# Kernel optimization log

Measured on AMD Instinct MI355X. Metric: run time of the kernel, lower is better.

The kernel has to match this reference:

```python
import jax, jax.numpy as jnp
import numpy as np

N = 100000        # nodes
E = 1600000       # edges (avg degree 16)
H = 128           # gnn_hidden_size
F_NODE = 4        # node_features (forced to 4 by _validate_and_fix_data)
F_EDGE = 2        # edge_features (forced to 2)
L = 3             # gnn_layers
BN_EPS = 1e-5
NORM_EPS = 1e-12


def _sage_layer(h, src, dst, eattr, Wn, Ws, gamma, beta):
    # message: lin_neighbor(concat(x_j, edge_attr)) where x_j = h[src]
    msg = jnp.concatenate([h[src], eattr], axis=-1) @ Wn          # [E+N, H]
    agg = jax.ops.segment_sum(msg, dst, num_segments=N)           # scatter-sum
    cnt = jax.ops.segment_sum(jnp.ones(dst.shape[0], h.dtype), dst, num_segments=N)
    agg = agg / jnp.maximum(cnt, 1.0)[:, None]                    # mean aggregation
    out = jax.nn.relu(agg + h @ Ws)                               # self-loop linear + ReLU
    # BatchNorm1d (batch statistics, biased var)
    mean = out.mean(axis=0)
    var = out.var(axis=0)
    out = (out - mean) * jax.lax.rsqrt(var + BN_EPS) * gamma + beta
    # dropout = identity (eval); L2 normalize per node
    nrm = jnp.maximum(jnp.linalg.norm(out, axis=-1, keepdims=True), NORM_EPS)
    return out / nrm


def setup_inputs() -> dict:
    key = jax.random.key(0)
    ks = jax.random.split(key, 24)
    s = 0.05
    inp = {
        "x": jax.random.normal(ks[0], (N, F_NODE), jnp.float32),
        "edge_index": jax.random.randint(ks[1], (2, E), 0, N, dtype=jnp.int32),
        "edge_attr": jax.random.uniform(ks[2], (E, F_EDGE), jnp.float32),
        "W_in": jax.random.normal(ks[3], (F_NODE, H), jnp.float32) * s,
        "b_in": jnp.zeros((H,), jnp.float32),
        "W_jump": jax.random.normal(ks[4], (L * H, H), jnp.float32) * s,
        "b_jump": jnp.zeros((H,), jnp.float32),
        "W1": jax.random.normal(ks[5], (H, H // 2), jnp.float32) * s,
        "b1": jnp.zeros((H // 2,), jnp.float32),
        "W2": jax.random.normal(ks[6], (H // 2, 1), jnp.float32) * s,
        "b2": jnp.zeros((1,), jnp.float32),
    }
    for l in range(L):
        inp[f"Wn_{l}"] = jax.random.normal(ks[7 + 4 * l], (H + F_EDGE, H), jnp.float32) * s
        inp[f"Ws_{l}"] = jax.random.normal(ks[8 + 4 * l], (H, H), jnp.float32) * s
        inp[f"gamma_{l}"] = jnp.ones((H,), jnp.float32)
        inp[f"beta_{l}"] = jnp.zeros((H,), jnp.float32)
    return inp


def reference(x, edge_index, edge_attr, W_in, b_in,
              Wn_0, Ws_0, gamma_0, beta_0,
              Wn_1, Ws_1, gamma_1, beta_1,
              Wn_2, Ws_2, gamma_2, beta_2,
              W_jump, b_jump, W1, b1, W2, b2):
    # add self loops (with zero edge_attr), as in _safe_add_self_loops
    loop = jnp.arange(N, dtype=edge_index.dtype)
    src = jnp.concatenate([edge_index[0], loop])
    dst = jnp.concatenate([edge_index[1], loop])
    eattr = jnp.concatenate([edge_attr, jnp.zeros((N, F_EDGE), edge_attr.dtype)], axis=0)

    h = x @ W_in + b_in                                          # input_projection
    layer_params = [(Wn_0, Ws_0, gamma_0, beta_0),
                    (Wn_1, Ws_1, gamma_1, beta_1),
                    (Wn_2, Ws_2, gamma_2, beta_2)]
    layer_outputs = []
    for Wn, Ws, gamma, beta in layer_params:
        h = _sage_layer(h, src, dst, eattr, Wn, Ws, gamma, beta)
        layer_outputs.append(h)
    # jump (skip) connection: concat all layer outputs -> Linear -> ReLU
    h = jax.nn.relu(jnp.concatenate(layer_outputs, axis=-1) @ W_jump + b_jump)
    # neighbor_scorer: Linear -> ReLU -> Linear -> scalar per node
    scores = jax.nn.relu(h @ W1 + b1) @ W2 + b2                  # [N, 1]
    return scores[:, 0]
```

## Files before the change

kernel.cpp:

```cpp
#include <hip/hip_runtime.h>


#define HDIM 128

using f16x8 = __attribute__((ext_vector_type(8))) _Float16;
using f32x4 = __attribute__((ext_vector_type(4))) float;

__device__ inline unsigned pack_f16x2(float a, float b) {
  _Float16 ha = (_Float16)a, hb = (_Float16)b;
  unsigned short ua = __builtin_bit_cast(unsigned short, ha);
  unsigned short ub = __builtin_bit_cast(unsigned short, hb);
  return (unsigned)ua | ((unsigned)ub << 16);
}
__device__ inline float2 unpack_f16x2(unsigned u) {
  _Float16 lo = __builtin_bit_cast(_Float16, (unsigned short)(u & 0xffffu));
  _Float16 hi = __builtin_bit_cast(_Float16, (unsigned short)(u >> 16));
  return make_float2((float)lo, (float)hi);
}

__global__ __launch_bounds__(256) void count_kernel(
    const int* __restrict__ dst, int* __restrict__ cnt,
    int* __restrict__ rank, int E) {
  int e = blockIdx.x * 256 + threadIdx.x;
  if (e >= E) return;
  rank[e] = atomicAdd(&cnt[dst[e]], 1);
}

__global__ __launch_bounds__(128) void scan_block_sum(
    const int* __restrict__ cnt, int* __restrict__ bsum, int N) {
  __shared__ int sd[128];
  int t = threadIdx.x;
  int i = blockIdx.x * 128 + t;
  sd[t] = (i < N) ? cnt[i] : 0;
  __syncthreads();
  for (int off = 64; off > 0; off >>= 1) {
    if (t < off) sd[t] += sd[t + off];
    __syncthreads();
  }
  if (t == 0) bsum[blockIdx.x] = sd[0];
}

__global__ __launch_bounds__(256) void scan_partials(
    const int* __restrict__ bsum, int* __restrict__ boff, int nch) {
  __shared__ int sd[256];
  int t = threadIdx.x;
  int base = t * 4;
  int v0 = (base + 0 < nch) ? bsum[base + 0] : 0;
  int v1 = (base + 1 < nch) ? bsum[base + 1] : 0;
  int v2 = (base + 2 < nch) ? bsum[base + 2] : 0;
  int v3 = (base + 3 < nch) ? bsum[base + 3] : 0;
  sd[t] = v0 + v1 + v2 + v3;
  __syncthreads();
  for (int off = 1; off < 256; off <<= 1) {
    int x = sd[t];
    int y = (t >= off) ? sd[t - off] : 0;
    __syncthreads();
    sd[t] = x + y;
    __syncthreads();
  }
  int run = (t == 0) ? 0 : sd[t - 1];
  if (base + 0 < nch) boff[base + 0] = run; run += v0;
  if (base + 1 < nch) boff[base + 1] = run; run += v1;
  if (base + 2 < nch) boff[base + 2] = run; run += v2;
  if (base + 3 < nch) boff[base + 3] = run;
}

__global__ __launch_bounds__(128) void scan_final(
    const int* __restrict__ cnt, const int* __restrict__ boff,
    int* __restrict__ rs, int N) {
  __shared__ int sd[128];
  int t = threadIdx.x, b = blockIdx.x;
  int i = b * 128 + t;
  int v = (i < N) ? cnt[i] : 0;
  sd[t] = v;
  __syncthreads();
  for (int off = 1; off < 128; off <<= 1) {
    int x = sd[t];
    int y = (t >= off) ? sd[t - off] : 0;
    __syncthreads();
    sd[t] = x + y;
    __syncthreads();
  }
  if (i < N) rs[i] = boff[b] + ((t == 0) ? 0 : sd[t - 1]);
}

__global__ __launch_bounds__(256) void fill_kernel(
    const int* __restrict__ src, const int* __restrict__ dst,
    const float* __restrict__ ea, const int* __restrict__ rs,
    const int* __restrict__ rank, uint2* __restrict__ cidx2, int E) {
  int e = blockIdx.x * 256 + threadIdx.x;
  if (e >= E) return;
  int d = dst[e];
  float2 v = *reinterpret_cast<const float2*>(&ea[2 * (size_t)e]);
  int pos = rs[d] + rank[e];
  cidx2[pos] = make_uint2((unsigned)src[e], pack_f16x2(v.x, v.y));
}

__global__ __launch_bounds__(256) void aggx_kernel(
    const float* __restrict__ x, const int* __restrict__ rs,
    const int* __restrict__ cnt, const uint2* __restrict__ cidx2,
    float* __restrict__ aggx, float* __restrict__ eagg, int N) {
  int i = blockIdx.x * 256 + threadIdx.x;
  if (i >= N) return;
  float4 a = *reinterpret_cast<const float4*>(&x[(size_t)i * 4]);
  float4 b = make_float4(0.f, 0.f, 0.f, 0.f);
  float e0 = 0.f, e1 = 0.f, f0 = 0.f, f1 = 0.f;
  int p = rs[i], e = p + cnt[i];
  for (; p + 1 < e; p += 2) {
    uint2 c0 = cidx2[p], c1 = cidx2[p + 1];
    float4 v0 = *reinterpret_cast<const float4*>(&x[(size_t)c0.x * 4]);
    float4 v1 = *reinterpret_cast<const float4*>(&x[(size_t)c1.x * 4]);
    float2 u0 = unpack_f16x2(c0.y);
    float2 u1 = unpack_f16x2(c1.y);
    a.x += v0.x; a.y += v0.y; a.z += v0.z; a.w += v0.w;
    b.x += v1.x; b.y += v1.y; b.z += v1.z; b.w += v1.w;
    e0 += u0.x; e1 += u0.y;
    f0 += u1.x; f1 += u1.y;
  }
  if (p < e) {
    uint2 c0 = cidx2[p];
    float4 v0 = *reinterpret_cast<const float4*>(&x[(size_t)c0.x * 4]);
    float2 u0 = unpack_f16x2(c0.y);
    a.x += v0.x; a.y += v0.y; a.z += v0.z; a.w += v0.w;
    e0 += u0.x; e1 += u0.y;
  }
  a.x += b.x; a.y += b.y; a.z += b.z; a.w += b.w;
  *reinterpret_cast<float4*>(&aggx[(size_t)i * 4]) = a;
  eagg[2 * (size_t)i + 0] = e0 + f0;
  eagg[2 * (size_t)i + 1] = e1 + f1;
}

__global__ __launch_bounds__(256) void pack_weights_kernel(
    const float* __restrict__ Wn0, const float* __restrict__ Ws0,
    const float* __restrict__ Wn1, const float* __restrict__ Ws1,
    const float* __restrict__ Wn2, const float* __restrict__ Ws2,
    const float* __restrict__ Wj, _Float16* __restrict__ outp) {
  int i = blockIdx.x * 256 + threadIdx.x;
  if (i >= 147456) return;
  int j = i & 7, lane = (i >> 3) & 63;
  float v;
  if (i < 98304) {
    int l = i >> 15;
    int r = i & 32767;
    int nt = (r >> 9) & 7, kt = r >> 12;
    int k = kt * 32 + (lane >> 4) * 8 + j;
    int n = nt * 16 + (lane & 15);
    const float* Wn = (l == 0) ? Wn0 : (l == 1) ? Wn1 : Wn2;
    const float* Ws = (l == 0) ? Ws0 : (l == 1) ? Ws1 : Ws2;
    v = (k < 128) ? Wn[(size_t)k * HDIM + n] : Ws[(size_t)(k - 128) * HDIM + n];
  } else {
    int r = i - 98304;
    int nt = (r >> 9) & 7, kt = r >> 12;
    int k = kt * 32 + (lane >> 4) * 8 + j;
    int n = nt * 16 + (lane & 15);
    v = Wj[(size_t)k * HDIM + n];
  }
  outp[i] = (_Float16)v;
}

template <bool L0>
__global__ __launch_bounds__(256) void sage_mfma_kernel(
    const float* __restrict__ A0f, const float* __restrict__ A1f,
    const _Float16* __restrict__ Hprev, const int* __restrict__ rs,
    const uint2* __restrict__ cidx2,
    const float* __restrict__ Wi, const float* __restrict__ bi,
    const float* __restrict__ eagg, const int* __restrict__ cnt,
    const _Float16* __restrict__ Bp, const float* __restrict__ Wn,
    _Float16* __restrict__ outh, float* __restrict__ bnstat, int N) {
  __shared__ _Float16 sA[64 * 256];
  __shared__ float sE[128];
  __shared__ float sBNs[4][128];
  __shared__ float sBNq[4][128];
  const int t = threadIdx.x;
  const int base = blockIdx.x * 64;

  if (t < 64) {
    int grow = base + t;
    float e0 = 0.f, e1 = 0.f;
    if (grow < N) {
      float inv = 1.0f / ((float)cnt[grow] + 1.0f);
      e0 = eagg[2 * (size_t)grow] * inv;
      e1 = eagg[2 * (size_t)grow + 1] * inv;
    }
    sE[2 * t] = e0;
    sE[2 * t + 1] = e1;
  }

  if (L0) {
#pragma unroll
    for (int it = 0; it < 8; ++it) {
      int c = t + it * 256;
      int row = c >> 5, k8 = c & 31;
      int grow = base + row;
      f16x8 hv = {};
      if (grow < N) {
        float inv = 1.0f / ((float)cnt[grow] + 1.0f);
        float scale = (k8 < 16) ? inv : 1.0f;
        const float* rp = (k8 < 16) ? &A0f[(size_t)grow * 4] : &A1f[(size_t)grow * 4];
        float4 r = *reinterpret_cast<const float4*>(rp);
        int col0 = (k8 & 15) * 8;
#pragma unroll
        for (int jj = 0; jj < 8; ++jj) {
          int col = col0 + jj;
          hv[jj] = (_Float16)(bi[col] + scale * (r.x * Wi[col] + r.y * Wi[HDIM + col] +
                                                 r.z * Wi[2 * HDIM + col] + r.w * Wi[3 * HDIM + col]));
        }
      }
      int byte = (row * 512 + k8 * 16) ^ ((row & 7) << 4);
      *reinterpret_cast<f16x8*>(reinterpret_cast<char*>(sA) + byte) = hv;
    }
  } else {
    const int row = t >> 2, q = t & 3;
    const int grow = base + row;
    float acc[32];
#pragma unroll
    for (int c = 0; c < 32; ++c) acc[c] = 0.f;
    f16x8 selfv[4] = {};
    if (grow < N) {
      const f16x8* selfp = reinterpret_cast<const f16x8*>(Hprev + (size_t)grow * HDIM) + q * 4;
#pragma unroll
      for (int j = 0; j < 4; ++j) {
        selfv[j] = selfp[j];
#pragma unroll
        for (int jj = 0; jj < 8; ++jj) acc[j * 8 + jj] = (float)selfv[j][jj];
      }
      int p = rs[grow];
      int e = p + cnt[grow];
      for (; p + 1 < e; p += 2) {
        uint2 q0 = cidx2[p], q1 = cidx2[p + 1];
        const f16x8* n0 = reinterpret_cast<const f16x8*>(Hprev + (size_t)q0.x * HDIM) + q * 4;
        const f16x8* n1 = reinterpret_cast<const f16x8*>(Hprev + (size_t)q1.x * HDIM) + q * 4;
        f16x8 c0[4], c1[4];
#pragma unroll
        for (int j = 0; j < 4; ++j) c0[j] = n0[j];
#pragma unroll
        for (int j = 0; j < 4; ++j) c1[j] = n1[j];
#pragma unroll
        for (int j = 0; j < 4; ++j)
#pragma unroll
          for (int jj = 0; jj < 8; ++jj)
            acc[j * 8 + jj] += (float)c0[j][jj] + (float)c1[j][jj];
      }
      if (p < e) {
        uint2 q0 = cidx2[p];
        const f16x8* n0 = reinterpret_cast<const f16x8*>(Hprev + (size_t)q0.x * HDIM) + q * 4;
#pragma unroll
        for (int j = 0; j < 4; ++j) {
          f16x8 c0 = n0[j];
#pragma unroll
          for (int jj = 0; jj < 8; ++jj) acc[j * 8 + jj] += (float)c0[jj];
        }
      }
      float inv = 1.0f / ((float)cnt[grow] + 1.0f);
#pragma unroll
      for (int c = 0; c < 32; ++c) acc[c] *= inv;
    }
    const int swz = (row & 7) << 4;
#pragma unroll
    for (int j = 0; j < 4; ++j) {
      f16x8 av;
#pragma unroll
      for (int jj = 0; jj < 8; ++jj) av[jj] = (_Float16)acc[j * 8 + jj];
      int k8a = q * 4 + j;
      *reinterpret_cast<f16x8*>(reinterpret_cast<char*>(sA) +
                                ((row * 512 + k8a * 16) ^ swz)) = av;
      int k8h = 16 + q * 4 + j;
      *reinterpret_cast<f16x8*>(reinterpret_cast<char*>(sA) +
                                ((row * 512 + k8h * 16) ^ swz)) = selfv[j];
    }
  }
  __syncthreads();

  const int lane = t & 63;
  const int w = t >> 6;
  const int col16 = lane & 15;
  const int kgrp = lane >> 4;
  f32x4 acc[8];
#pragma unroll
  for (int nt = 0; nt < 8; ++nt) acc[nt] = (f32x4){0.f, 0.f, 0.f, 0.f};

  const int arow = w * 16 + col16;
  const int aswz = (arow & 7) << 4;
#pragma unroll
  for (int kt = 0; kt < 8; ++kt) {
    int abyte = (arow * 512 + kt * 64 + kgrp * 16) ^ aswz;
    f16x8 a = *reinterpret_cast<const f16x8*>(reinterpret_cast<const char*>(sA) + abyte);
    const f16x8* bp = reinterpret_cast<const f16x8*>(Bp) + (size_t)kt * 512 + lane;
#pragma unroll
    for (int nt = 0; nt < 8; ++nt) {
      f16x8 b = bp[nt * 64];
      acc[nt] = __builtin_amdgcn_mfma_f32_16x16x32_f16(a, b, acc[nt], 0, 0, 0);
    }
  }

#pragma unroll
  for (int nt = 0; nt < 8; ++nt) {
    int col = nt * 16 + col16;
    float we0 = Wn[(size_t)128 * HDIM + col];
    float we1 = Wn[(size_t)129 * HDIM + col];
    float s = 0.f, q = 0.f;
#pragma unroll
    for (int i = 0; i < 4; ++i) {
      int lr = w * 16 + kgrp * 4 + i;
      int row = base + lr;
      if (row < N) {
        float v = acc[nt][i] + sE[2 * lr] * we0 + sE[2 * lr + 1] * we1;
        v = fmaxf(v, 0.f);
        outh[(size_t)row * HDIM + col] = (_Float16)v;
        s += v;
        q += v * v;
      }
    }
    s += __shfl_xor(s, 16, 64);
    s += __shfl_xor(s, 32, 64);
    q += __shfl_xor(q, 16, 64);
    q += __shfl_xor(q, 32, 64);
    if (lane < 16) {
      sBNs[w][col] = s;
      sBNq[w][col] = q;
    }
  }
  __syncthreads();
  if (t < 128) {
    float s = sBNs[0][t] + sBNs[1][t] + sBNs[2][t] + sBNs[3][t];
    float q = sBNq[0][t] + sBNq[1][t] + sBNq[2][t] + sBNq[3][t];
    atomicAdd(&bnstat[t], s);
    atomicAdd(&bnstat[HDIM + t], q);
  }
}

__global__ __launch_bounds__(256) void bn_l2_kernel(
    const _Float16* __restrict__ outh, const float* __restrict__ stat,
    const float* __restrict__ gamma, const float* __restrict__ beta,
    float invN, _Float16* __restrict__ h, int N) {
  __shared__ float sAB[256];
  int t = threadIdx.x;
  if (t < 128) {
    float mean = stat[t] * invN;
    float var = stat[128 + t] * invN - mean * mean;
    float A = gamma[t] / sqrtf(var + 1e-5f);
    sAB[t] = A;
    sAB[128 + t] = beta[t] - mean * A;
  }
  __syncthreads();
  int i = blockIdx.x * 4 + (t >> 6);
  if (i >= N) return;
  int lane = t & 63;
  unsigned u = (reinterpret_cast<const unsigned*>(outh + (size_t)i * HDIM))[lane];
  float2 v = unpack_f16x2(u);
  float A0 = sAB[lane * 2 + 0], A1 = sAB[lane * 2 + 1];
  float B0 = sAB[128 + lane * 2 + 0], B1 = sAB[128 + lane * 2 + 1];
  float y0 = v.x * A0 + B0;
  float y1 = v.y * A1 + B1;
  float s = y0 * y0 + y1 * y1;
#pragma unroll
  for (int m = 32; m > 0; m >>= 1) s += __shfl_xor(s, m, 64);
  float inv = 1.0f / fmaxf(sqrtf(s), 1e-12f);
  (reinterpret_cast<unsigned*>(h + (size_t)i * HDIM))[lane] =
      pack_f16x2(y0 * inv, y1 * inv);
}

__global__ __launch_bounds__(256) void jump_mfma_kernel(
    const _Float16* __restrict__ h1, const _Float16* __restrict__ h2,
    const _Float16* __restrict__ h3, const _Float16* __restrict__ Bp,
    const float* __restrict__ bj, const float* __restrict__ W1p,
    const float* __restrict__ b1p, const float* __restrict__ W2p,
    const float* __restrict__ b2p, float* __restrict__ outp, int N) {
  __shared__ _Float16 sA[64 * 384];
  const int t = threadIdx.x;
  const int base = blockIdx.x * 64;

  const _Float16* hs[3] = {h1, h2, h3};
#pragma unroll
  for (int it = 0; it < 12; ++it) {
    int c = t + it * 256;
    int row = c / 48, k8 = c % 48;
    int grow = base + row;
    f16x8 hv = {};
    if (grow < N)
      hv = (reinterpret_cast<const f16x8*>(hs[k8 >> 4] + (size_t)grow * HDIM))[k8 & 15];
    int byte = (row * 768 + k8 * 16) ^ ((row & 7) << 4);
    *reinterpret_cast<f16x8*>(reinterpret_cast<char*>(sA) + byte) = hv;
  }
  __syncthreads();

  const int lane = t & 63;
  const int w = t >> 6;
  const int col16 = lane & 15;
  const int kgrp = lane >> 4;
  f32x4 acc[8];
#pragma unroll
  for (int nt = 0; nt < 8; ++nt) acc[nt] = (f32x4){0.f, 0.f, 0.f, 0.f};

  const int arow = w * 16 + col16;
  const int aswz = (arow & 7) << 4;
#pragma unroll
  for (int kt = 0; kt < 12; ++kt) {
    int abyte = (arow * 768 + kt * 64 + kgrp * 16) ^ aswz;
    f16x8 a = *reinterpret_cast<const f16x8*>(reinterpret_cast<const char*>(sA) + abyte);
    const f16x8* bp = reinterpret_cast<const f16x8*>(Bp) + (size_t)kt * 512 + lane;
#pragma unroll
    for (int nt = 0; nt < 8; ++nt) {
      f16x8 b = bp[nt * 64];
      acc[nt] = __builtin_amdgcn_mfma_f32_16x16x32_f16(a, b, acc[nt], 0, 0, 0);
    }
  }
  __syncthreads();

  float* sG = reinterpret_cast<float*>(sA);
  float* sS = sG + 64 * 128;
#pragma unroll
  for (int nt = 0; nt < 8; ++nt) {
    int col = nt * 16 + col16;
    float bb = bj[col];
#pragma unroll
    for (int i = 0; i < 4; ++i) {
      int lr = w * 16 + kgrp * 4 + i;
      sG[lr * 128 + col] = fmaxf(acc[nt][i] + bb, 0.f);
    }
  }
  __syncthreads();

  const int m = t & 63, grp = t >> 6;
  float a2[16];
#pragma unroll
  for (int i = 0; i < 16; ++i) a2[i] = b1p[m];
#pragma unroll 4
  for (int k = 0; k < 128; ++k) {
    float wv = W1p[(size_t)k * 64 + m];
#pragma unroll
    for (int i = 0; i < 16; ++i) a2[i] += sG[(grp * 16 + i) * 128 + k] * wv;
  }
#pragma unroll
  for (int i = 0; i < 16; ++i) sS[(grp * 16 + i) * 64 + m] = fmaxf(a2[i], 0.f);
  __syncthreads();

  if (t < 64) {
    int row = base + t;
    if (row < N) {
      float s = b2p[0];
#pragma unroll 8
      for (int mm = 0; mm < 64; ++mm) s += sS[t * 64 + mm] * W2p[mm];
      outp[row] = s;
    }
  }
}

extern "C" void kernel_launch(void* const* d_in, const int* in_sizes, int n_in,
                              void* d_out, int out_size, void* d_ws, size_t ws_size,
                              hipStream_t stream) {
  const float* x      = (const float*)d_in[0];
  const int*   ei     = (const int*)d_in[1];
  const float* eattr  = (const float*)d_in[2];
  const float* W_in   = (const float*)d_in[3];
  const float* b_in   = (const float*)d_in[4];
  const float* W_jump = (const float*)d_in[5];
  const float* b_jump = (const float*)d_in[6];
  const float* W1     = (const float*)d_in[7];
  const float* b1     = (const float*)d_in[8];
  const float* W2     = (const float*)d_in[9];
  const float* b2     = (const float*)d_in[10];
  const float* Wn[3] = {(const float*)d_in[11], (const float*)d_in[15], (const float*)d_in[19]};
  const float* Ws[3] = {(const float*)d_in[12], (const float*)d_in[16], (const float*)d_in[20]};
  const float* gm[3] = {(const float*)d_in[13], (const float*)d_in[17], (const float*)d_in[21]};
  const float* bt[3] = {(const float*)d_in[14], (const float*)d_in[18], (const float*)d_in[22]};

  const int N = in_sizes[0] / 4;
  const int E = in_sizes[2] / 2;
  const int* srcp = ei;
  const int* dstp = ei + (size_t)E;
  const int nch = (N + 127) / 128;
  const size_t nh = (size_t)N * HDIM;

  char* wsb = (char*)d_ws;
  size_t off = 0;
  auto carve = [&](size_t bytes) -> void* {
    void* p = wsb + off;
    off = (off + bytes + 255) & ~(size_t)255;
    return p;
  };
  _Float16* h1   = (_Float16*)carve(nh * 2);
  _Float16* h2   = (_Float16*)carve(nh * 2);
  _Float16* h3   = (_Float16*)carve(nh * 2);
  _Float16* outh = (_Float16*)carve(nh * 2);
  float*    aggx = (float*)carve((size_t)N * 4 * 4);
  float*    eagg = (float*)carve((size_t)N * 2 * 4);
  int*      cnt  = (int*)carve((size_t)N * 4);
  int*      rowstart = (int*)carve((size_t)N * 4);
  int*      rank     = (int*)carve((size_t)E * 4);
  uint2*    cidx2    = (uint2*)carve((size_t)E * 8);
  int*      bsum = (int*)carve(4096);
  int*      boff = (int*)carve(4096);
  float*    bnstat = (float*)carve(1024);
  _Float16* wpack  = (_Float16*)carve(147456 * 2);

  hipMemsetAsync(cnt, 0, (size_t)N * sizeof(int), stream);
  count_kernel<<<(E + 255) / 256, 256, 0, stream>>>(dstp, cnt, rank, E);
  pack_weights_kernel<<<(147456 + 255) / 256, 256, 0, stream>>>(
      Wn[0], Ws[0], Wn[1], Ws[1], Wn[2], Ws[2], W_jump, wpack);
  scan_block_sum<<<nch, 128, 0, stream>>>(cnt, bsum, N);
  scan_partials<<<1, 256, 0, stream>>>(bsum, boff, nch);
  scan_final<<<nch, 128, 0, stream>>>(cnt, boff, rowstart, N);
  fill_kernel<<<(E + 255) / 256, 256, 0, stream>>>(srcp, dstp, eattr, rowstart, rank, cidx2, E);

  const int gemm_grid = (N + 63) / 64;
  const float invN = 1.0f / (float)N;

  aggx_kernel<<<(N + 255) / 256, 256, 0, stream>>>(x, rowstart, cnt, cidx2, aggx, eagg, N);
  hipMemsetAsync(bnstat, 0, 256 * sizeof(float), stream);
  sage_mfma_kernel<true><<<gemm_grid, 256, 0, stream>>>(
      aggx, x, nullptr, rowstart, cidx2, W_in, b_in, eagg, cnt, wpack, Wn[0],
      outh, bnstat, N);
  bn_l2_kernel<<<(N + 3) / 4, 256, 0, stream>>>(outh, bnstat, gm[0], bt[0], invN, h1, N);

  _Float16* hbuf[3] = {h1, h2, h3};
  for (int l = 1; l < 3; ++l) {
    hipMemsetAsync(bnstat, 0, 256 * sizeof(float), stream);
    sage_mfma_kernel<false><<<gemm_grid, 256, 0, stream>>>(
        nullptr, nullptr, hbuf[l - 1], rowstart, cidx2, nullptr, nullptr, eagg, cnt,
        wpack + (size_t)l * 32768, Wn[l], outh, bnstat, N);
    bn_l2_kernel<<<(N + 3) / 4, 256, 0, stream>>>(outh, bnstat, gm[l], bt[l], invN, hbuf[l], N);
  }

  jump_mfma_kernel<<<gemm_grid, 256, 0, stream>>>(h1, h2, h3, wpack + 98304, b_jump,
                                                  W1, b1, W2, b2, (float*)d_out, N);
}
```

Baseline: 590.7 us.

## Restructure neighbor gather to half-wave per row with deeper unrolling

The aggregation phase of the SAGE kernel is remapped so that 32 lanes cooperatively load one 256-byte neighbor row as f16x4 pieces. Two rows are processed per wave, and up to 8 neighbor gathers are kept in flight per iteration. The old mapping had 4 threads per row, each loading 64 bytes with only 2 neighbors unrolled. Blocks shrink to 128 threads covering 32 rows, and each wave now fills only its own 16 MFMA rows, which lets the non-layer-0 path drop the block barrier. The aim is more memory-level parallelism and better-coalesced gathers, at the cost of more blocks and twice as many BN-stat atomics.

Measured after the change: 651.9 us. 1.1x slower.

```diff
diff --git a/kernel.cpp b/kernel.cpp
--- a/kernel.cpp
+++ b/kernel.cpp
@@ -4,6 +4,7 @@
 #define HDIM 128
 
 using f16x8 = __attribute__((ext_vector_type(8))) _Float16;
+using f16x4 = __attribute__((ext_vector_type(4))) _Float16;
 using f32x4 = __attribute__((ext_vector_type(4))) float;
 
 __device__ inline unsigned pack_f16x2(float a, float b) {
@@ -159,7 +160,7 @@
 }
 
 template <bool L0>
-__global__ __launch_bounds__(256) void sage_mfma_kernel(
+__global__ __launch_bounds__(128, 4) void sage_mfma_kernel(
     const float* __restrict__ A0f, const float* __restrict__ A1f,
     const _Float16* __restrict__ Hprev, const int* __restrict__ rs,
     const uint2* __restrict__ cidx2,
@@ -167,29 +168,32 @@
     const float* __restrict__ eagg, const int* __restrict__ cnt,
     const _Float16* __restrict__ Bp, const float* __restrict__ Wn,
     _Float16* __restrict__ outh, float* __restrict__ bnstat, int N) {
-  __shared__ _Float16 sA[64 * 256];
-  __shared__ float sE[128];
-  __shared__ float sBNs[4][128];
-  __shared__ float sBNq[4][128];
+  __shared__ _Float16 sA[32 * 256];
+  __shared__ float sE[64];
+  __shared__ float sBNs[2][128];
+  __shared__ float sBNq[2][128];
   const int t = threadIdx.x;
-  const int base = blockIdx.x * 64;
-
-  if (t < 64) {
-    int grow = base + t;
+  const int w = t >> 6;
+  const int lane = t & 63;
+  const int base = blockIdx.x * 32;
+
+  if (lane < 16) {
+    int row = w * 16 + lane;
+    int grow = base + row;
     float e0 = 0.f, e1 = 0.f;
     if (grow < N) {
       float inv = 1.0f / ((float)cnt[grow] + 1.0f);
       e0 = eagg[2 * (size_t)grow] * inv;
       e1 = eagg[2 * (size_t)grow + 1] * inv;
     }
-    sE[2 * t] = e0;
-    sE[2 * t + 1] = e1;
+    sE[2 * row] = e0;
+    sE[2 * row + 1] = e1;
   }
 
   if (L0) {
 #pragma unroll
     for (int it = 0; it < 8; ++it) {
-      int c = t + it * 256;
+      int c = t + it * 128;
       int row = c >> 5, k8 = c & 31;
       int grow = base + row;
       f16x8 hv = {};
@@ -209,70 +213,74 @@
       int byte = (row * 512 + k8 * 16) ^ ((row & 7) << 4);
       *reinterpret_cast<f16x8*>(reinterpret_cast<char*>(sA) + byte) = hv;
     }
+    __syncthreads();
   } else {
-    const int row = t >> 2, q = t & 3;
-    const int grow = base + row;
-    float acc[32];
-#pragma unroll
-    for (int c = 0; c < 32; ++c) acc[c] = 0.f;
-    f16x8 selfv[4] = {};
-    if (grow < N) {
-      const f16x8* selfp = reinterpret_cast<const f16x8*>(Hprev + (size_t)grow * HDIM) + q * 4;
-#pragma unroll
-      for (int j = 0; j < 4; ++j) {
-        selfv[j] = selfp[j];
-#pragma unroll
-        for (int jj = 0; jj < 8; ++jj) acc[j * 8 + jj] = (float)selfv[j][jj];
+    const int sub = lane >> 5;
+    const int sl = lane & 31;
+    const f16x4* hb = reinterpret_cast<const f16x4*>(Hprev) + sl;
+    char* sAb = reinterpret_cast<char*>(sA);
+#pragma unroll 2
+    for (int rp = 0; rp < 8; ++rp) {
+      int row = w * 16 + rp * 2 + sub;
+      int grow = base + row;
+      float a0 = 0.f, a1 = 0.f, a2 = 0.f, a3 = 0.f;
+      f16x4 selfv = {};
+      if (grow < N) {
+        selfv = hb[(size_t)grow * 32];
+        a0 = (float)selfv[0]; a1 = (float)selfv[1];
+        a2 = (float)selfv[2]; a3 = (float)selfv[3];
+        int p = rs[grow];
+        const int cn = cnt[grow];
+        int e = p + cn;
+        for (; p + 7 < e; p += 8) {
+          uint2 q0 = cidx2[p], q1 = cidx2[p + 1], q2 = cidx2[p + 2], q3 = cidx2[p + 3];
+          uint2 q4 = cidx2[p + 4], q5 = cidx2[p + 5], q6 = cidx2[p + 6], q7 = cidx2[p + 7];
+          f16x4 v0 = hb[(size_t)q0.x * 32];
+          f16x4 v1 = hb[(size_t)q1.x * 32];
+          f16x4 v2 = hb[(size_t)q2.x * 32];
+          f16x4 v3 = hb[(size_t)q3.x * 32];
+          f16x4 v4 = hb[(size_t)q4.x * 32];
+          f16x4 v5 = hb[(size_t)q5.x * 32];
+          f16x4 v6 = hb[(size_t)q6.x * 32];
+          f16x4 v7 = hb[(size_t)q7.x * 32];
+          a0 += (float)v0[0] + (float)v1[0] + (float)v2[0] + (float)v3[0] +
+                (float)v4[0] + (float)v5[0] + (float)v6[0] + (float)v7[0];
+          a1 += (float)v0[1] + (float)v1[1] + (float)v2[1] + (float)v3[1] +
+                (float)v4[1] + (float)v5[1] + (float)v6[1] + (float)v7[1];
+          a2 += (float)v0[2] + (float)v1[2] + (float)v2[2] + (float)v3[2] +
+                (float)v4[2] + (float)v5[2] + (float)v6[2] + (float)v7[2];
+          a3 += (float)v0[3] + (float)v1[3] + (float)v2[3] + (float)v3[3] +
+                (float)v4[3] + (float)v5[3] + (float)v6[3] + (float)v7[3];
+        }
+        for (; p + 3 < e; p += 4) {
+          uint2 q0 = cidx2[p], q1 = cidx2[p + 1], q2 = cidx2[p + 2], q3 = cidx2[p + 3];
+          f16x4 v0 = hb[(size_t)q0.x * 32];
+          f16x4 v1 = hb[(size_t)q1.x * 32];
+          f16x4 v2 = hb[(size_t)q2.x * 32];
+          f16x4 v3 = hb[(size_t)q3.x * 32];
+          a0 += (float)v0[0] + (float)v1[0] + (float)v2[0] + (float)v3[0];
+          a1 += (float)v0[1] + (float)v1[1] + (float)v2[1] + (float)v3[1];
+          a2 += (float)v0[2] + (float)v1[2] + (float)v2[2] + (float)v3[2];
+          a3 += (float)v0[3] + (float)v1[3] + (float)v2[3] + (float)v3[3];
+        }
+        for (; p < e; ++p) {
+          uint2 q0 = cidx2[p];
+          f16x4 v0 = hb[(size_t)q0.x * 32];
+          a0 += (float)v0[0]; a1 += (float)v0[1];
+          a2 += (float)v0[2]; a3 += (float)v0[3];
+        }
+        float inv = 1.0f / ((float)cn + 1.0f);
+        a0 *= inv; a1 *= inv; a2 *= inv; a3 *= inv;
       }
-      int p = rs[grow];
-      int e = p + cnt[grow];
-      for (; p + 1 < e; p += 2) {
-        uint2 q0 = cidx2[p], q1 = cidx2[p + 1];
-        const f16x8* n0 = reinterpret_cast<const f16x8*>(Hprev + (size_t)q0.x * HDIM) + q * 4;
-        const f16x8* n1 = reinterpret_cast<const f16x8*>(Hprev + (size_t)q1.x * HDIM) + q * 4;
-        f16x8 c0[4], c1[4];
-#pragma unroll
-        for (int j = 0; j < 4; ++j) c0[j] = n0[j];
-#pragma unroll
-        for (int j = 0; j < 4; ++j) c1[j] = n1[j];
-#pragma unroll
-        for (int j = 0; j < 4; ++j)
-#pragma unroll
-          for (int jj = 0; jj < 8; ++jj)
-            acc[j * 8 + jj] += (float)c0[j][jj] + (float)c1[j][jj];
-      }
-      if (p < e) {
-        uint2 q0 = cidx2[p];
-        const f16x8* n0 = reinterpret_cast<const f16x8*>(Hprev + (size_t)q0.x * HDIM) + q * 4;
-#pragma unroll
-        for (int j = 0; j < 4; ++j) {
-          f16x8 c0 = n0[j];
-#pragma unroll
-          for (int jj = 0; jj < 8; ++jj) acc[j * 8 + jj] += (float)c0[jj];
-        }
-      }
-      float inv = 1.0f / ((float)cnt[grow] + 1.0f);
-#pragma unroll
-      for (int c = 0; c < 32; ++c) acc[c] *= inv;
-    }
-    const int swz = (row & 7) << 4;
-#pragma unroll
-    for (int j = 0; j < 4; ++j) {
-      f16x8 av;
-#pragma unroll
-      for (int jj = 0; jj < 8; ++jj) av[jj] = (_Float16)acc[j * 8 + jj];
-      int k8a = q * 4 + j;
-      *reinterpret_cast<f16x8*>(reinterpret_cast<char*>(sA) +
-                                ((row * 512 + k8a * 16) ^ swz)) = av;
-      int k8h = 16 + q * 4 + j;
-      *reinterpret_cast<f16x8*>(reinterpret_cast<char*>(sA) +
-                                ((row * 512 + k8h * 16) ^ swz)) = selfv[j];
-    }
-  }
-  __syncthreads();
-
-  const int lane = t & 63;
-  const int w = t >> 6;
+      int swz = (row & 7) << 4;
+      f16x4 av;
+      av[0] = (_Float16)a0; av[1] = (_Float16)a1;
+      av[2] = (_Float16)a2; av[3] = (_Float16)a3;
+      *reinterpret_cast<f16x4*>(sAb + ((row * 512 + sl * 8) ^ swz)) = av;
+      *reinterpret_cast<f16x4*>(sAb + ((row * 512 + 256 + sl * 8) ^ swz)) = selfv;
+    }
+  }
+
   const int col16 = lane & 15;
   const int kgrp = lane >> 4;
   f32x4 acc[8];
@@ -322,8 +330,8 @@
   }
   __syncthreads();
   if (t < 128) {
-    float s = sBNs[0][t] + sBNs[1][t] + sBNs[2][t] + sBNs[3][t];
-    float q = sBNq[0][t] + sBNq[1][t] + sBNq[2][t] + sBNq[3][t];
+    float s = sBNs[0][t] + sBNs[1][t];
+    float q = sBNq[0][t] + sBNq[1][t];
     atomicAdd(&bnstat[t], s);
     atomicAdd(&bnstat[HDIM + t], q);
   }
@@ -503,12 +511,12 @@
   scan_final<<<nch, 128, 0, stream>>>(cnt, boff, rowstart, N);
   fill_kernel<<<(E + 255) / 256, 256, 0, stream>>>(srcp, dstp, eattr, rowstart, rank, cidx2, E);
 
-  const int gemm_grid = (N + 63) / 64;
+  const int sage_grid = (N + 31) / 32;
   const float invN = 1.0f / (float)N;
 
   aggx_kernel<<<(N + 255) / 256, 256, 0, stream>>>(x, rowstart, cnt, cidx2, aggx, eagg, N);
   hipMemsetAsync(bnstat, 0, 256 * sizeof(float), stream);
-  sage_mfma_kernel<true><<<gemm_grid, 256, 0, stream>>>(
+  sage_mfma_kernel<true><<<sage_grid, 128, 0, stream>>>(
       aggx, x, nullptr, rowstart, cidx2, W_in, b_in, eagg, cnt, wpack, Wn[0],
       outh, bnstat, N);
   bn_l2_kernel<<<(N + 3) / 4, 256, 0, stream>>>(outh, bnstat, gm[0], bt[0], invN, h1, N);
@@ -516,12 +524,12 @@
   _Float16* hbuf[3] = {h1, h2, h3};
   for (int l = 1; l < 3; ++l) {
     hipMemsetAsync(bnstat, 0, 256 * sizeof(float), stream);
-    sage_mfma_kernel<false><<<gemm_grid, 256, 0, stream>>>(
+    sage_mfma_kernel<false><<<sage_grid, 128, 0, stream>>>(
         nullptr, nullptr, hbuf[l - 1], rowstart, cidx2, nullptr, nullptr, eagg, cnt,
         wpack + (size_t)l * 32768, Wn[l], outh, bnstat, N);
     bn_l2_kernel<<<(N + 3) / 4, 256, 0, stream>>>(outh, bnstat, gm[l], bt[l], invN, hbuf[l], N);
   }
 
-  jump_mfma_kernel<<<gemm_grid, 256, 0, stream>>>(h1, h2, h3, wpack + 98304, b_jump,
-                                                  W1, b1, W2, b2, (float*)d_out, N);
-}
+  jump_mfma_kernel<<<(N + 63) / 64, 256, 0, stream>>>(h1, h2, h3, wpack + 98304, b_jump,
+                                                      W1, b1, W2, b2, (float*)d_out, N);
+}
```

## Split neighbor gather into column-chunked kernel over transposed feature layout

Applied to the files above, without the earlier changes.

Node features are now stored in a chunk-transposed layout, with 8 chunks of 16 fp16 columns each. A new gather kernel aggregates neighbors one chunk at a time, so each chunk pass touches a 3.2 MB slice that can stay in cache, and it reads a compact int-only neighbor index. The SAGE GEMM kernel then only loads the precomputed mean aggregate and the self features, and the BN and jump kernels are adapted to the new layout. This adds an extra kernel launch per layer plus an extra aggregate buffer write and read, and the index array is read eight times.

Measured after the change: 740.3 us. 25.3% more time.

```diff
diff --git a/kernel.cpp b/kernel.cpp
--- a/kernel.cpp
+++ b/kernel.cpp
@@ -87,13 +87,16 @@
 __global__ __launch_bounds__(256) void fill_kernel(
     const int* __restrict__ src, const int* __restrict__ dst,
     const float* __restrict__ ea, const int* __restrict__ rs,
-    const int* __restrict__ rank, uint2* __restrict__ cidx2, int E) {
+    const int* __restrict__ rank, uint2* __restrict__ cidx2,
+    int* __restrict__ cidx1, int E) {
   int e = blockIdx.x * 256 + threadIdx.x;
   if (e >= E) return;
   int d = dst[e];
+  int s = src[e];
   float2 v = *reinterpret_cast<const float2*>(&ea[2 * (size_t)e]);
   int pos = rs[d] + rank[e];
-  cidx2[pos] = make_uint2((unsigned)src[e], pack_f16x2(v.x, v.y));
+  cidx2[pos] = make_uint2((unsigned)s, pack_f16x2(v.x, v.y));
+  cidx1[pos] = s;
 }
 
 __global__ __launch_bounds__(256) void aggx_kernel(
@@ -128,6 +131,61 @@
   *reinterpret_cast<float4*>(&aggx[(size_t)i * 4]) = a;
   eagg[2 * (size_t)i + 0] = e0 + f0;
   eagg[2 * (size_t)i + 1] = e1 + f1;
+}
+
+__global__ __launch_bounds__(256) void gatherT_kernel(
+    const _Float16* __restrict__ hT, const int* __restrict__ rs,
+    const int* __restrict__ cnt, const int* __restrict__ cidx1,
+    _Float16* __restrict__ aggT, int N) {
+  const int c = blockIdx.x & 7;
+  const int i = (blockIdx.x >> 3) * 256 + threadIdx.x;
+  if (i >= N) return;
+  const f16x8* hb = reinterpret_cast<const f16x8*>(hT) + (size_t)c * N * 2;
+  f16x8 s0 = hb[(size_t)i * 2];
+  f16x8 s1 = hb[(size_t)i * 2 + 1];
+  float acc[16];
+#pragma unroll
+  for (int j = 0; j < 8; ++j) {
+    acc[j] = (float)s0[j];
+    acc[8 + j] = (float)s1[j];
+  }
+  int p = rs[i];
+  const int cn = cnt[i];
+  int e = p + cn;
+  for (; p + 3 < e; p += 4) {
+    int n0 = __builtin_nontemporal_load(cidx1 + p);
+    int n1 = __builtin_nontemporal_load(cidx1 + p + 1);
+    int n2 = __builtin_nontemporal_load(cidx1 + p + 2);
+    int n3 = __builtin_nontemporal_load(cidx1 + p + 3);
+    f16x8 a0 = hb[(size_t)n0 * 2], a1 = hb[(size_t)n0 * 2 + 1];
+    f16x8 b0 = hb[(size_t)n1 * 2], b1 = hb[(size_t)n1 * 2 + 1];
+    f16x8 c0 = hb[(size_t)n2 * 2], c1 = hb[(size_t)n2 * 2 + 1];
+    f16x8 d0 = hb[(size_t)n3 * 2], d1 = hb[(size_t)n3 * 2 + 1];
+#pragma unroll
+    for (int j = 0; j < 8; ++j) {
+      acc[j] += ((float)a0[j] + (float)b0[j]) + ((float)c0[j] + (float)d0[j]);
+      acc[8 + j] += ((float)a1[j] + (float)b1[j]) + ((float)c1[j] + (float)d1[j]);
+    }
+  }
+  for (; p < e; ++p) {
+    int n0 = __builtin_nontemporal_load(cidx1 + p);
+    f16x8 a0 = hb[(size_t)n0 * 2], a1 = hb[(size_t)n0 * 2 + 1];
+#pragma unroll
+    for (int j = 0; j < 8; ++j) {
+      acc[j] += (float)a0[j];
+      acc[8 + j] += (float)a1[j];
+    }
+  }
+  float inv = 1.0f / ((float)cn + 1.0f);
+  f16x8 o0, o1;
+#pragma unroll
+  for (int j = 0; j < 8; ++j) {
+    o0[j] = (_Float16)(acc[j] * inv);
+    o1[j] = (_Float16)(acc[8 + j] * inv);
+  }
+  f16x8* op = reinterpret_cast<f16x8*>(aggT) + (size_t)c * N * 2 + (size_t)i * 2;
+  __builtin_nontemporal_store(o0, op);
+  __builtin_nontemporal_store(o1, op + 1);
 }
 
 __global__ __launch_bounds__(256) void pack_weights_kernel(
@@ -161,8 +219,7 @@
 template <bool L0>
 __global__ __launch_bounds__(256) void sage_mfma_kernel(
     const float* __restrict__ A0f, const float* __restrict__ A1f,
-    const _Float16* __restrict__ Hprev, const int* __restrict__ rs,
-    const uint2* __restrict__ cidx2,
+    const _Float16* __restrict__ AggT, const _Float16* __restrict__ HprevT,
     const float* __restrict__ Wi, const float* __restrict__ bi,
     const float* __restrict__ eagg, const int* __restrict__ cnt,
     const _Float16* __restrict__ Bp, const float* __restrict__ Wn,
@@ -210,63 +267,20 @@
       *reinterpret_cast<f16x8*>(reinterpret_cast<char*>(sA) + byte) = hv;
     }
   } else {
-    const int row = t >> 2, q = t & 3;
-    const int grow = base + row;
-    float acc[32];
-#pragma unroll
-    for (int c = 0; c < 32; ++c) acc[c] = 0.f;
-    f16x8 selfv[4] = {};
-    if (grow < N) {
-      const f16x8* selfp = reinterpret_cast<const f16x8*>(Hprev + (size_t)grow * HDIM) + q * 4;
-#pragma unroll
-      for (int j = 0; j < 4; ++j) {
-        selfv[j] = selfp[j];
-#pragma unroll
-        for (int jj = 0; jj < 8; ++jj) acc[j * 8 + jj] = (float)selfv[j][jj];
+#pragma unroll
+    for (int it = 0; it < 8; ++it) {
+      int idx = it * 256 + t;
+      int row = idx & 63, k8 = idx >> 6;
+      int grow = base + row;
+      f16x8 hv = {};
+      if (grow < N) {
+        int k = k8 & 15;
+        const _Float16* srcp = (k8 < 16) ? AggT : HprevT;
+        hv = *reinterpret_cast<const f16x8*>(
+            srcp + ((size_t)(k >> 1) * N + grow) * 16 + (k & 1) * 8);
       }
-      int p = rs[grow];
-      int e = p + cnt[grow];
-      for (; p + 1 < e; p += 2) {
-        uint2 q0 = cidx2[p], q1 = cidx2[p + 1];
-        const f16x8* n0 = reinterpret_cast<const f16x8*>(Hprev + (size_t)q0.x * HDIM) + q * 4;
-        const f16x8* n1 = reinterpret_cast<const f16x8*>(Hprev + (size_t)q1.x * HDIM) + q * 4;
-        f16x8 c0[4], c1[4];
-#pragma unroll
-        for (int j = 0; j < 4; ++j) c0[j] = n0[j];
-#pragma unroll
-        for (int j = 0; j < 4; ++j) c1[j] = n1[j];
-#pragma unroll
-        for (int j = 0; j < 4; ++j)
-#pragma unroll
-          for (int jj = 0; jj < 8; ++jj)
-            acc[j * 8 + jj] += (float)c0[j][jj] + (float)c1[j][jj];
-      }
-      if (p < e) {
-        uint2 q0 = cidx2[p];
-        const f16x8* n0 = reinterpret_cast<const f16x8*>(Hprev + (size_t)q0.x * HDIM) + q * 4;
-#pragma unroll
-        for (int j = 0; j < 4; ++j) {
-          f16x8 c0 = n0[j];
-#pragma unroll
-          for (int jj = 0; jj < 8; ++jj) acc[j * 8 + jj] += (float)c0[jj];
-        }
-      }
-      float inv = 1.0f / ((float)cnt[grow] + 1.0f);
-#pragma unroll
-      for (int c = 0; c < 32; ++c) acc[c] *= inv;
-    }
-    const int swz = (row & 7) << 4;
-#pragma unroll
-    for (int j = 0; j < 4; ++j) {
-      f16x8 av;
-#pragma unroll
-      for (int jj = 0; jj < 8; ++jj) av[jj] = (_Float16)acc[j * 8 + jj];
-      int k8a = q * 4 + j;
-      *reinterpret_cast<f16x8*>(reinterpret_cast<char*>(sA) +
-                                ((row * 512 + k8a * 16) ^ swz)) = av;
-      int k8h = 16 + q * 4 + j;
-      *reinterpret_cast<f16x8*>(reinterpret_cast<char*>(sA) +
-                                ((row * 512 + k8h * 16) ^ swz)) = selfv[j];
+      int byte = (row * 512 + k8 * 16) ^ ((row & 7) << 4);
+      *reinterpret_cast<f16x8*>(reinterpret_cast<char*>(sA) + byte) = hv;
     }
   }
   __syncthreads();
@@ -332,7 +346,7 @@
 __global__ __launch_bounds__(256) void bn_l2_kernel(
     const _Float16* __restrict__ outh, const float* __restrict__ stat,
     const float* __restrict__ gamma, const float* __restrict__ beta,
-    float invN, _Float16* __restrict__ h, int N) {
+    float invN, _Float16* __restrict__ hT, int N) {
   __shared__ float sAB[256];
   int t = threadIdx.x;
   if (t < 128) {
@@ -356,8 +370,8 @@
 #pragma unroll
   for (int m = 32; m > 0; m >>= 1) s += __shfl_xor(s, m, 64);
   float inv = 1.0f / fmaxf(sqrtf(s), 1e-12f);
-  (reinterpret_cast<unsigned*>(h + (size_t)i * HDIM))[lane] =
-      pack_f16x2(y0 * inv, y1 * inv);
+  size_t off = ((size_t)(lane >> 3) * N + i) * 16 + (lane & 7) * 2;
+  *reinterpret_cast<unsigned*>(hT + off) = pack_f16x2(y0 * inv, y1 * inv);
 }
 
 __global__ __launch_bounds__(256) void jump_mfma_kernel(
@@ -373,12 +387,15 @@
   const _Float16* hs[3] = {h1, h2, h3};
 #pragma unroll
   for (int it = 0; it < 12; ++it) {
-    int c = t + it * 256;
-    int row = c / 48, k8 = c % 48;
+    int idx = it * 256 + t;
+    int row = idx & 63, k8 = idx >> 6;
     int grow = base + row;
     f16x8 hv = {};
-    if (grow < N)
-      hv = (reinterpret_cast<const f16x8*>(hs[k8 >> 4] + (size_t)grow * HDIM))[k8 & 15];
+    if (grow < N) {
+      int kk = k8 & 15;
+      hv = *reinterpret_cast<const f16x8*>(
+          hs[k8 >> 4] + ((size_t)(kk >> 1) * N + grow) * 16 + (kk & 1) * 8);
+    }
     int byte = (row * 768 + k8 * 16) ^ ((row & 7) << 4);
     *reinterpret_cast<f16x8*>(reinterpret_cast<char*>(sA) + byte) = hv;
   }
@@ -483,12 +500,14 @@
   _Float16* h2   = (_Float16*)carve(nh * 2);
   _Float16* h3   = (_Float16*)carve(nh * 2);
   _Float16* outh = (_Float16*)carve(nh * 2);
+  _Float16* aggT = (_Float16*)carve(nh * 2);
   float*    aggx = (float*)carve((size_t)N * 4 * 4);
   float*    eagg = (float*)carve((size_t)N * 2 * 4);
   int*      cnt  = (int*)carve((size_t)N * 4);
   int*      rowstart = (int*)carve((size_t)N * 4);
   int*      rank     = (int*)carve((size_t)E * 4);
   uint2*    cidx2    = (uint2*)carve((size_t)E * 8);
+  int*      cidx1    = (int*)carve((size_t)E * 4);
   int*      bsum = (int*)carve(4096);
   int*      boff = (int*)carve(4096);
   float*    bnstat = (float*)carve(1024);
@@ -501,23 +520,26 @@
   scan_block_sum<<<nch, 128, 0, stream>>>(cnt, bsum, N);
   scan_partials<<<1, 256, 0, stream>>>(bsum, boff, nch);
   scan_final<<<nch, 128, 0, stream>>>(cnt, boff, rowstart, N);
-  fill_kernel<<<(E + 255) / 256, 256, 0, stream>>>(srcp, dstp, eattr, rowstart, rank, cidx2, E);
+  fill_kernel<<<(E + 255) / 256, 256, 0, stream>>>(srcp, dstp, eattr, rowstart, rank,
+                                                   cidx2, cidx1, E);
 
   const int gemm_grid = (N + 63) / 64;
+  const int gat_grid = 8 * ((N + 255) / 256);
   const float invN = 1.0f / (float)N;
 
   aggx_kernel<<<(N + 255) / 256, 256, 0, stream>>>(x, rowstart, cnt, cidx2, aggx, eagg, N);
   hipMemsetAsync(bnstat, 0, 256 * sizeof(float), stream);
   sage_mfma_kernel<true><<<gemm_grid, 256, 0, stream>>>(
-      aggx, x, nullptr, rowstart, cidx2, W_in, b_in, eagg, cnt, wpack, Wn[0],
+      aggx, x, nullptr, nullptr, W_in, b_in, eagg, cnt, wpack, Wn[0],
       outh, bnstat, N);
   bn_l2_kernel<<<(N + 3) / 4, 256, 0, stream>>>(outh, bnstat, gm[0], bt[0], invN, h1, N);
 
   _Float16* hbuf[3] = {h1, h2, h3};
   for (int l = 1; l < 3; ++l) {
+    gatherT_kernel<<<gat_grid, 256, 0, stream>>>(hbuf[l - 1], rowstart, cnt, cidx1, aggT, N);
     hipMemsetAsync(bnstat, 0, 256 * sizeof(float), stream);
     sage_mfma_kernel<false><<<gemm_grid, 256, 0, stream>>>(
-        nullptr, nullptr, hbuf[l - 1], rowstart, cidx2, nullptr, nullptr, eagg, cnt,
+        nullptr, nullptr, aggT, hbuf[l - 1], nullptr, nullptr, eagg, cnt,
         wpack + (size_t)l * 32768, Wn[l], outh, bnstat, N);
     bn_l2_kernel<<<(N + 3) / 4, 256, 0, stream>>>(outh, bnstat, gm[l], bt[l], invN, hbuf[l], N);
   }
```

## Sort CSR neighbor lists by source-index bucket for gather locality

Applied to the files above, without the earlier changes.

Counting is now done per (destination, source bucket) pair with 16 buckets of 8192 source ids. Each row's neighbors in the CSR are therefore grouped by source range, so the layer gather kernels read Hprev rows in roughly ascending address order, which should improve cache locality. The scan now covers 16N entries, a rowmeta kernel derives per-node counts, and the gather loop walks the 16 bucket boundaries. BN stat buffers are split per layer so one memset replaces three, in exchange for a heavier preprocessing scan and extra bounds reads in the inner loop.

Measured after the change: 710.4 us. 20.3% more time.

```diff
diff --git a/kernel.cpp b/kernel.cpp
--- a/kernel.cpp
+++ b/kernel.cpp
@@ -18,22 +18,35 @@
   return make_float2((float)lo, (float)hi);
 }
 
+__device__ inline int src_bucket(int s) {
+  int b = s >> 13;
+  return (b > 15) ? 15 : b;
+}
+
 __global__ __launch_bounds__(256) void count_kernel(
-    const int* __restrict__ dst, int* __restrict__ cnt,
-    int* __restrict__ rank, int E) {
+    const int* __restrict__ src, const int* __restrict__ dst,
+    int* __restrict__ cnt16, int* __restrict__ rank, int E) {
   int e = blockIdx.x * 256 + threadIdx.x;
   if (e >= E) return;
-  rank[e] = atomicAdd(&cnt[dst[e]], 1);
-}
-
-__global__ __launch_bounds__(128) void scan_block_sum(
-    const int* __restrict__ cnt, int* __restrict__ bsum, int N) {
-  __shared__ int sd[128];
+  int d = dst[e];
+  int s = src[e];
+  rank[e] = atomicAdd(&cnt16[((size_t)d << 4) + src_bucket(s)], 1);
+}
+
+__global__ __launch_bounds__(256) void scan_block_sum2048(
+    const int* __restrict__ a, int* __restrict__ bsum, int M) {
+  __shared__ int sd[256];
   int t = threadIdx.x;
-  int i = blockIdx.x * 128 + t;
-  sd[t] = (i < N) ? cnt[i] : 0;
-  __syncthreads();
-  for (int off = 64; off > 0; off >>= 1) {
+  int base = blockIdx.x * 2048 + t * 8;
+  int s = 0;
+#pragma unroll
+  for (int j = 0; j < 8; ++j) {
+    int i = base + j;
+    s += (i < M) ? a[i] : 0;
+  }
+  sd[t] = s;
+  __syncthreads();
+  for (int off = 128; off > 0; off >>= 1) {
     if (t < off) sd[t] += sd[t + off];
     __syncthreads();
   }
@@ -65,39 +78,63 @@
   if (base + 3 < nch) boff[base + 3] = run;
 }
 
-__global__ __launch_bounds__(128) void scan_final(
-    const int* __restrict__ cnt, const int* __restrict__ boff,
-    int* __restrict__ rs, int N) {
-  __shared__ int sd[128];
-  int t = threadIdx.x, b = blockIdx.x;
-  int i = b * 128 + t;
-  int v = (i < N) ? cnt[i] : 0;
-  sd[t] = v;
-  __syncthreads();
-  for (int off = 1; off < 128; off <<= 1) {
+__global__ __launch_bounds__(256) void scan_final2048(
+    const int* __restrict__ a, const int* __restrict__ boff,
+    int* __restrict__ outp, int M) {
+  __shared__ int sd[256];
+  int t = threadIdx.x;
+  int base = blockIdx.x * 2048 + t * 8;
+  int v[8];
+  int s = 0;
+#pragma unroll
+  for (int j = 0; j < 8; ++j) {
+    int i = base + j;
+    v[j] = (i < M) ? a[i] : 0;
+    s += v[j];
+  }
+  sd[t] = s;
+  __syncthreads();
+  for (int off = 1; off < 256; off <<= 1) {
     int x = sd[t];
     int y = (t >= off) ? sd[t - off] : 0;
     __syncthreads();
     sd[t] = x + y;
     __syncthreads();
   }
-  if (i < N) rs[i] = boff[b] + ((t == 0) ? 0 : sd[t - 1]);
+  int run = boff[blockIdx.x] + ((t == 0) ? 0 : sd[t - 1]);
+#pragma unroll
+  for (int j = 0; j < 8; ++j) {
+    int i = base + j;
+    if (i < M) outp[i] = run;
+    run += v[j];
+  }
+}
+
+__global__ __launch_bounds__(256) void rowmeta_kernel(
+    int* __restrict__ rs16, int* __restrict__ cnt, int N, int E) {
+  int i = blockIdx.x * 256 + threadIdx.x;
+  if (i >= N) return;
+  int start = rs16[(size_t)i << 4];
+  int end = (i == N - 1) ? E : rs16[((size_t)i << 4) + 16];
+  cnt[i] = end - start;
+  if (i == N - 1) rs16[(size_t)N << 4] = E;
 }
 
 __global__ __launch_bounds__(256) void fill_kernel(
     const int* __restrict__ src, const int* __restrict__ dst,
-    const float* __restrict__ ea, const int* __restrict__ rs,
+    const float* __restrict__ ea, const int* __restrict__ rs16,
     const int* __restrict__ rank, uint2* __restrict__ cidx2, int E) {
   int e = blockIdx.x * 256 + threadIdx.x;
   if (e >= E) return;
   int d = dst[e];
+  int s = src[e];
   float2 v = *reinterpret_cast<const float2*>(&ea[2 * (size_t)e]);
-  int pos = rs[d] + rank[e];
-  cidx2[pos] = make_uint2((unsigned)src[e], pack_f16x2(v.x, v.y));
+  int pos = rs16[((size_t)d << 4) + src_bucket(s)] + rank[e];
+  cidx2[pos] = make_uint2((unsigned)s, pack_f16x2(v.x, v.y));
 }
 
 __global__ __launch_bounds__(256) void aggx_kernel(
-    const float* __restrict__ x, const int* __restrict__ rs,
+    const float* __restrict__ x, const int* __restrict__ rs16,
     const int* __restrict__ cnt, const uint2* __restrict__ cidx2,
     float* __restrict__ aggx, float* __restrict__ eagg, int N) {
   int i = blockIdx.x * 256 + threadIdx.x;
@@ -105,7 +142,7 @@
   float4 a = *reinterpret_cast<const float4*>(&x[(size_t)i * 4]);
   float4 b = make_float4(0.f, 0.f, 0.f, 0.f);
   float e0 = 0.f, e1 = 0.f, f0 = 0.f, f1 = 0.f;
-  int p = rs[i], e = p + cnt[i];
+  int p = rs16[(size_t)i << 4], e = p + cnt[i];
   for (; p + 1 < e; p += 2) {
     uint2 c0 = cidx2[p], c1 = cidx2[p + 1];
     float4 v0 = *reinterpret_cast<const float4*>(&x[(size_t)c0.x * 4]);
@@ -161,7 +198,7 @@
 template <bool L0>
 __global__ __launch_bounds__(256) void sage_mfma_kernel(
     const float* __restrict__ A0f, const float* __restrict__ A1f,
-    const _Float16* __restrict__ Hprev, const int* __restrict__ rs,
+    const _Float16* __restrict__ Hprev, const int* __restrict__ rs16,
     const uint2* __restrict__ cidx2,
     const float* __restrict__ Wi, const float* __restrict__ bi,
     const float* __restrict__ eagg, const int* __restrict__ cnt,
@@ -224,31 +261,35 @@
 #pragma unroll
         for (int jj = 0; jj < 8; ++jj) acc[j * 8 + jj] = (float)selfv[j][jj];
       }
-      int p = rs[grow];
-      int e = p + cnt[grow];
-      for (; p + 1 < e; p += 2) {
-        uint2 q0 = cidx2[p], q1 = cidx2[p + 1];
-        const f16x8* n0 = reinterpret_cast<const f16x8*>(Hprev + (size_t)q0.x * HDIM) + q * 4;
-        const f16x8* n1 = reinterpret_cast<const f16x8*>(Hprev + (size_t)q1.x * HDIM) + q * 4;
-        f16x8 c0[4], c1[4];
-#pragma unroll
-        for (int j = 0; j < 4; ++j) c0[j] = n0[j];
-#pragma unroll
-        for (int j = 0; j < 4; ++j) c1[j] = n1[j];
-#pragma unroll
-        for (int j = 0; j < 4; ++j)
-#pragma unroll
-          for (int jj = 0; jj < 8; ++jj)
-            acc[j * 8 + jj] += (float)c0[j][jj] + (float)c1[j][jj];
-      }
-      if (p < e) {
-        uint2 q0 = cidx2[p];
-        const f16x8* n0 = reinterpret_cast<const f16x8*>(Hprev + (size_t)q0.x * HDIM) + q * 4;
-#pragma unroll
-        for (int j = 0; j < 4; ++j) {
-          f16x8 c0 = n0[j];
-#pragma unroll
-          for (int jj = 0; jj < 8; ++jj) acc[j * 8 + jj] += (float)c0[jj];
+      const int rbase = grow << 4;
+      int p = rs16[rbase];
+      for (int b = 1; b <= 16; ++b) {
+        int pe = rs16[rbase + b];
+        for (; p + 1 < pe; p += 2) {
+          uint2 q0 = cidx2[p], q1 = cidx2[p + 1];
+          const f16x8* m0 = reinterpret_cast<const f16x8*>(Hprev + (size_t)q0.x * HDIM) + q * 4;
+          const f16x8* m1 = reinterpret_cast<const f16x8*>(Hprev + (size_t)q1.x * HDIM) + q * 4;
+          f16x8 c0[4], c1[4];
+#pragma unroll
+          for (int j = 0; j < 4; ++j) c0[j] = m0[j];
+#pragma unroll
+          for (int j = 0; j < 4; ++j) c1[j] = m1[j];
+#pragma unroll
+          for (int j = 0; j < 4; ++j)
+#pragma unroll
+            for (int jj = 0; jj < 8; ++jj)
+              acc[j * 8 + jj] += (float)c0[j][jj] + (float)c1[j][jj];
+        }
+        if (p < pe) {
+          uint2 q0 = cidx2[p];
+          const f16x8* m0 = reinterpret_cast<const f16x8*>(Hprev + (size_t)q0.x * HDIM) + q * 4;
+#pragma unroll
+          for (int j = 0; j < 4; ++j) {
+            f16x8 c0 = m0[j];
+#pragma unroll
+            for (int jj = 0; jj < 8; ++jj) acc[j * 8 + jj] += (float)c0[jj];
+          }
+          p = pe;
         }
       }
       float inv = 1.0f / ((float)cnt[grow] + 1.0f);
@@ -469,8 +510,9 @@
   const int E = in_sizes[2] / 2;
   const int* srcp = ei;
   const int* dstp = ei + (size_t)E;
-  const int nch = (N + 127) / 128;
   const size_t nh = (size_t)N * HDIM;
+  const int M = 16 * N;
+  const int nch = (M + 2047) / 2048;
 
   char* wsb = (char*)d_ws;
   size_t off = 0;
@@ -486,40 +528,42 @@
   float*    aggx = (float*)carve((size_t)N * 4 * 4);
   float*    eagg = (float*)carve((size_t)N * 2 * 4);
   int*      cnt  = (int*)carve((size_t)N * 4);
-  int*      rowstart = (int*)carve((size_t)N * 4);
-  int*      rank     = (int*)carve((size_t)E * 4);
-  uint2*    cidx2    = (uint2*)carve((size_t)E * 8);
+  int*      cnt16 = (int*)carve((size_t)M * 4);
+  int*      rs16  = (int*)carve(((size_t)M + 16) * 4);
+  int*      rank  = (int*)carve((size_t)E * 4);
+  uint2*    cidx2 = (uint2*)carve((size_t)E * 8);
   int*      bsum = (int*)carve(4096);
   int*      boff = (int*)carve(4096);
-  float*    bnstat = (float*)carve(1024);
+  float*    bnstat = (float*)carve(3 * 256 * sizeof(float));
   _Float16* wpack  = (_Float16*)carve(147456 * 2);
 
-  hipMemsetAsync(cnt, 0, (size_t)N * sizeof(int), stream);
-  count_kernel<<<(E + 255) / 256, 256, 0, stream>>>(dstp, cnt, rank, E);
+  hipMemsetAsync(cnt16, 0, (size_t)M * sizeof(int), stream);
+  hipMemsetAsync(bnstat, 0, 3 * 256 * sizeof(float), stream);
+  count_kernel<<<(E + 255) / 256, 256, 0, stream>>>(srcp, dstp, cnt16, rank, E);
   pack_weights_kernel<<<(147456 + 255) / 256, 256, 0, stream>>>(
       Wn[0], Ws[0], Wn[1], Ws[1], Wn[2], Ws[2], W_jump, wpack);
-  scan_block_sum<<<nch, 128, 0, stream>>>(cnt, bsum, N);
+  scan_block_sum2048<<<nch, 256, 0, stream>>>(cnt16, bsum, M);
   scan_partials<<<1, 256, 0, stream>>>(bsum, boff, nch);
-  scan_final<<<nch, 128, 0, stream>>>(cnt, boff, rowstart, N);
-  fill_kernel<<<(E + 255) / 256, 256, 0, stream>>>(srcp, dstp, eattr, rowstart, rank, cidx2, E);
+  scan_final2048<<<nch, 256, 0, stream>>>(cnt16, boff, rs16, M);
+  rowmeta_kernel<<<(N + 255) / 256, 256, 0, stream>>>(rs16, cnt, N, E);
+  fill_kernel<<<(E + 255) / 256, 256, 0, stream>>>(srcp, dstp, eattr, rs16, rank, cidx2, E);
 
   const int gemm_grid = (N + 63) / 64;
   const float invN = 1.0f / (float)N;
 
-  aggx_kernel<<<(N + 255) / 256, 256, 0, stream>>>(x, rowstart, cnt, cidx2, aggx, eagg, N);
-  hipMemsetAsync(bnstat, 0, 256 * sizeof(float), stream);
+  aggx_kernel<<<(N + 255) / 256, 256, 0, stream>>>(x, rs16, cnt, cidx2, aggx, eagg, N);
   sage_mfma_kernel<true><<<gemm_grid, 256, 0, stream>>>(
-      aggx, x, nullptr, rowstart, cidx2, W_in, b_in, eagg, cnt, wpack, Wn[0],
+      aggx, x, nullptr, rs16, cidx2, W_in, b_in, eagg, cnt, wpack, Wn[0],
       outh, bnstat, N);
   bn_l2_kernel<<<(N + 3) / 4, 256, 0, stream>>>(outh, bnstat, gm[0], bt[0], invN, h1, N);
 
   _Float16* hbuf[3] = {h1, h2, h3};
   for (int l = 1; l < 3; ++l) {
-    hipMemsetAsync(bnstat, 0, 256 * sizeof(float), stream);
     sage_mfma_kernel<false><<<gemm_grid, 256, 0, stream>>>(
-        nullptr, nullptr, hbuf[l - 1], rowstart, cidx2, nullptr, nullptr, eagg, cnt,
-        wpack + (size_t)l * 32768, Wn[l], outh, bnstat, N);
-    bn_l2_kernel<<<(N + 3) / 4, 256, 0, stream>>>(outh, bnstat, gm[l], bt[l], invN, hbuf[l], N);
+        nullptr, nullptr, hbuf[l - 1], rs16, cidx2, nullptr, nullptr, eagg, cnt,
+        wpack + (size_t)l * 32768, Wn[l], outh, bnstat + 256 * l, N);
+    bn_l2_kernel<<<(N + 3) / 4, 256, 0, stream>>>(outh, bnstat + 256 * l,
+                                                  gm[l], bt[l], invN, hbuf[l], N);
   }
 
   jump_mfma_kernel<<<gemm_grid, 256, 0, stream>>>(h1, h2, h3, wpack + 98304, b_jump,
```
